# Kernel optimization log

Measured on AMD Instinct MI355X. Metric: run time of the kernel, lower is better.

The kernel has to match this reference:

```python
import jax, jax.numpy as jnp
import numpy as np

SAMPLE_RATE = 24000.0
SIGMA_MULT = 4.0
CHUNK = 512  # atoms processed per scan step (mirrors chunked Triton kernel)


def setup_inputs() -> dict:
    key = jax.random.key(0)
    ks = jax.random.split(key, 6)
    N = 4096
    num_samples = 72000  # 3 seconds at 24kHz
    duration = num_samples / SAMPLE_RATE
    amplitude = 0.1 * jax.random.normal(ks[0], (N,), dtype=jnp.float32)
    tau = jax.random.uniform(ks[1], (N,), dtype=jnp.float32) * duration
    omega = jax.random.uniform(ks[2], (N,), dtype=jnp.float32) * 8000.0
    sigma = 0.002 + jax.random.uniform(ks[3], (N,), dtype=jnp.float32) * 0.020
    phi = jax.random.uniform(ks[4], (N,), dtype=jnp.float32) * (2.0 * np.pi)
    gamma = 500.0 * jax.random.normal(ks[5], (N,), dtype=jnp.float32)
    return {"amplitude": amplitude, "tau": tau, "omega": omega,
            "sigma": sigma, "phi": phi, "gamma": gamma,
            "num_samples": num_samples}


def _render(amplitude, tau, omega, sigma, phi, gamma, num_samples):
    t = jnp.arange(num_samples, dtype=jnp.float32) / SAMPLE_RATE  # [T]
    two_pi = jnp.float32(2.0 * np.pi)

    def chunk_sum(acc, params):
        a, tu, om, sg, ph, gm = params  # each [CHUNK]
        tc = t[None, :] - tu[:, None]                    # [C,T]
        mask = jnp.abs(tc) <= SIGMA_MULT * sg[:, None]
        env = jnp.exp(-tc * tc / (2.0 * sg[:, None] ** 2 + 1e-8))
        phase = two_pi * (om[:, None] * tc + 0.5 * gm[:, None] * tc * tc) + ph[:, None]
        atoms = a[:, None] * env * jnp.cos(phase) * mask.astype(jnp.float32)
        return acc + atoms.sum(axis=0), None

    N = amplitude.shape[0]
    rs = lambda x: x.reshape(N // CHUNK, CHUNK)
    params = (rs(amplitude), rs(tau), rs(omega), rs(sigma), rs(phi), rs(gamma))
    out, _ = jax.lax.scan(chunk_sum, jnp.zeros((num_samples,), jnp.float32), params)
    return out


def reference(amplitude, tau, omega, sigma, phi, gamma, num_samples):
    return _render(amplitude, tau, omega, sigma, phi, gamma, num_samples)
```

## Files before the change

### kernel.cpp

```cpp
#include <hip/hip_runtime.h>
#include <math.h>


#define SR         24000.0f
#define TWO_PI     6.2831853071795864769f
#define LOG2E      1.4426950408889634f

#define TS     512
#define RBLOCK 128
#define SPT    4
#define SEGS   8
#define MAXA   512

__global__ __launch_bounds__(64) void prep_kernel(
        const float* __restrict__ tau,
        const float* __restrict__ sigma,
        int*   __restrict__ counts,
        int*   __restrict__ lists,
        float* __restrict__ out,
        int N, int T, int ntiles) {
    const int b    = blockIdx.x;
    const int lane = threadIdx.x;

    if (b < ntiles) {
        const float tstart = (float)(b * TS) * (1.0f / SR);
        const float tend   = (float)(b * TS + TS - 1) * (1.0f / SR);
        const float slack  = 2.0f / SR;
        int cnt = 0;
        for (int c = 0; c < N; c += 64) {
            const int ai = c + lane;
            bool hit = false;
            if (ai < N) {
                const float tu = tau[ai];
                const float w  = 4.0f * sigma[ai] + slack;
                hit = ((tu - w) <= tend) && ((tu + w) >= tstart);
            }
            const unsigned long long m = __ballot(hit);
            if (hit) {
                const int pos = cnt + (int)__popcll(m & ((1ull << lane) - 1ull));
                if (pos < MAXA) lists[b * MAXA + pos] = ai;
            }
            cnt += (int)__popcll(m);
        }
        if (lane == 0) counts[b] = (cnt < MAXA) ? cnt : MAXA;
    } else {
        const int i4 = (b - ntiles) * 64 + lane;
        if (i4 * 4 < T) ((float4*)out)[i4] = make_float4(0.f, 0.f, 0.f, 0.f);
    }
}

__global__ __launch_bounds__(RBLOCK) void render_kernel(
        const float* __restrict__ amp,
        const float* __restrict__ tau,
        const float* __restrict__ omega,
        const float* __restrict__ sigma,
        const float* __restrict__ phi,
        const float* __restrict__ gamma,
        const int*   __restrict__ counts,
        const int*   __restrict__ lists,
        float*       __restrict__ out,
        int T) {
    __shared__ float4 s_par[RBLOCK][2];

    const int tile = blockIdx.x;
    const int seg  = blockIdx.y;
    const int tid  = threadIdx.x;
    const int s_base = tile * TS;
    const float t0 = (float)(s_base + tid) * (1.0f / SR);
    const float dt = (float)RBLOCK * (1.0f / SR);

    int cnt = counts[tile];
    const int per = (cnt + SEGS - 1) / SEGS;
    const int a0 = seg * per;
    const int a1 = min(cnt, a0 + per);

    const int* lst = lists + tile * MAXA;
    float acc[SPT] = {0.0f, 0.0f, 0.0f, 0.0f};

    for (int base = a0; base < a1; base += RBLOCK) {
        const int m = min(RBLOCK, a1 - base);
        __syncthreads();
        if (tid < m) {
            const int idx = lst[base + tid];
            const float a  = amp[idx];
            const float tu = tau[idx];
            const float om = omega[idx];
            const float sg = sigma[idx];
            const float ph = phi[idx];
            const float gm = gamma[idx];
            const float k  = -LOG2E / (2.0f * sg * sg + 1e-8f);
            s_par[tid][0] = make_float4(a, tu, om, 0.5f * gm);
            s_par[tid][1] = make_float4(k, ph * (1.0f / TWO_PI), 0.0f, 0.0f);
        }
        __syncthreads();

        for (int i = 0; i < m; ++i) {
            const float4 p0 = s_par[i][0];
            const float4 p1 = s_par[i][1];
            const float tc0 = t0 - p0.y;
            #pragma unroll
            for (int j = 0; j < SPT; ++j) {
                const float tc  = tc0 + (float)j * dt;
                const float tc2 = tc * tc;
                const float env = exp2f(p1.x * tc2);
                const float rev = fmaf(p0.z, tc, fmaf(p0.w, tc2, p1.y));
                const float r   = rev - floorf(rev);
                const float c   = __builtin_amdgcn_cosf(r);
                acc[j] = fmaf(p0.x * env, c, acc[j]);
            }
        }
    }

    #pragma unroll
    for (int j = 0; j < SPT; ++j) {
        const int t_idx = s_base + tid + j * RBLOCK;
        if (t_idx < T && a1 > a0) atomicAdd(&out[t_idx], acc[j]);
    }
}

extern "C" void kernel_launch(void* const* d_in, const int* in_sizes, int n_in,
                              void* d_out, int out_size, void* d_ws, size_t ws_size,
                              hipStream_t stream) {
    const float* amp   = (const float*)d_in[0];
    const float* tau   = (const float*)d_in[1];
    const float* omega = (const float*)d_in[2];
    const float* sigma = (const float*)d_in[3];
    const float* phi   = (const float*)d_in[4];
    const float* gamma = (const float*)d_in[5];

    float* out = (float*)d_out;
    const int T = out_size;
    const int N = in_sizes[0];
    const int ntiles = (T + TS - 1) / TS;

    char* ws = (char*)d_ws;
    int* counts = (int*)ws;
    int* lists  = (int*)(ws + (size_t)ntiles * sizeof(int));

    const int zblocks = (T / 4 + 63) / 64;
    prep_kernel<<<ntiles + zblocks, 64, 0, stream>>>(tau, sigma, counts, lists,
                                                     out, N, T, ntiles);
    dim3 grid(ntiles, SEGS);
    render_kernel<<<grid, RBLOCK, 0, stream>>>(amp, tau, omega, sigma, phi, gamma,
                                               counts, lists, out, T);
}
```

Before: 95.94 us.

## Fuse atom binning and rendering into one kernel without atomics

Merges the prep (per-tile atom culling plus output zeroing) and render kernels into one kernel. Each 512-thread block culls all atoms for its tile with a block-wide ballot and prefix sum into shared memory, loads parameters, then has each thread render one sample and write it directly. This drops the second launch, the global lists buffer, the output zeroing and the atomicAdds. In exchange each tile's atom list is no longer split across 8 segment blocks, so only about 141 blocks run, each scanning all N atoms serially with barriers per chunk.

```diff
diff --git a/kernel.cpp b/kernel.cpp
--- a/kernel.cpp
+++ b/kernel.cpp
@@ -2,120 +2,96 @@
 #include <math.h>
 
 
-#define SR         24000.0f
-#define TWO_PI     6.2831853071795864769f
-#define LOG2E      1.4426950408889634f
+#define SR      24000.0f
+#define TWO_PI  6.2831853071795864769f
+#define LOG2E   1.4426950408889634f
 
-#define TS     512
-#define RBLOCK 128
-#define SPT    4
-#define SEGS   8
-#define MAXA   512
+#define TS      512
+#define BLK     512
+#define NWAVES  (BLK / 64)
+#define MAXA    512
 
-__global__ __launch_bounds__(64) void prep_kernel(
-        const float* __restrict__ tau,
-        const float* __restrict__ sigma,
-        int*   __restrict__ counts,
-        int*   __restrict__ lists,
-        float* __restrict__ out,
-        int N, int T, int ntiles) {
-    const int b    = blockIdx.x;
-    const int lane = threadIdx.x;
-
-    if (b < ntiles) {
-        const float tstart = (float)(b * TS) * (1.0f / SR);
-        const float tend   = (float)(b * TS + TS - 1) * (1.0f / SR);
-        const float slack  = 2.0f / SR;
-        int cnt = 0;
-        for (int c = 0; c < N; c += 64) {
-            const int ai = c + lane;
-            bool hit = false;
-            if (ai < N) {
-                const float tu = tau[ai];
-                const float w  = 4.0f * sigma[ai] + slack;
-                hit = ((tu - w) <= tend) && ((tu + w) >= tstart);
-            }
-            const unsigned long long m = __ballot(hit);
-            if (hit) {
-                const int pos = cnt + (int)__popcll(m & ((1ull << lane) - 1ull));
-                if (pos < MAXA) lists[b * MAXA + pos] = ai;
-            }
-            cnt += (int)__popcll(m);
-        }
-        if (lane == 0) counts[b] = (cnt < MAXA) ? cnt : MAXA;
-    } else {
-        const int i4 = (b - ntiles) * 64 + lane;
-        if (i4 * 4 < T) ((float4*)out)[i4] = make_float4(0.f, 0.f, 0.f, 0.f);
-    }
-}
-
-__global__ __launch_bounds__(RBLOCK) void render_kernel(
+__global__ __launch_bounds__(BLK) void gabor_fused_kernel(
         const float* __restrict__ amp,
         const float* __restrict__ tau,
         const float* __restrict__ omega,
         const float* __restrict__ sigma,
         const float* __restrict__ phi,
         const float* __restrict__ gamma,
-        const int*   __restrict__ counts,
-        const int*   __restrict__ lists,
         float*       __restrict__ out,
-        int T) {
-    __shared__ float4 s_par[RBLOCK][2];
+        int N, int T) {
+    __shared__ int    s_list[MAXA];
+    __shared__ int    s_wcnt[NWAVES];
+    __shared__ float4 s_p4[MAXA];
+    __shared__ float2 s_p2[MAXA];
 
     const int tile = blockIdx.x;
-    const int seg  = blockIdx.y;
     const int tid  = threadIdx.x;
-    const int s_base = tile * TS;
-    const float t0 = (float)(s_base + tid) * (1.0f / SR);
-    const float dt = (float)RBLOCK * (1.0f / SR);
+    const int wid  = tid >> 6;
+    const int lane = tid & 63;
 
-    int cnt = counts[tile];
-    const int per = (cnt + SEGS - 1) / SEGS;
-    const int a0 = seg * per;
-    const int a1 = min(cnt, a0 + per);
+    const float tstart = (float)(tile * TS) * (1.0f / SR);
+    const float tend   = (float)(tile * TS + TS - 1) * (1.0f / SR);
+    const float slack  = 2.0f / SR;
 
-    const int* lst = lists + tile * MAXA;
-    float acc[SPT] = {0.0f, 0.0f, 0.0f, 0.0f};
+    int total = 0;
+    for (int c = 0; c < N; c += BLK) {
+        const int ai = c + tid;
+        bool hit = false;
+        if (ai < N) {
+            const float tu = tau[ai];
+            const float w  = 4.0f * sigma[ai] + slack;
+            hit = ((tu - w) <= tend) && ((tu + w) >= tstart);
+        }
+        const unsigned long long m = __ballot(hit);
+        if (lane == 0) s_wcnt[wid] = (int)__popcll(m);
+        __syncthreads();
 
-    for (int base = a0; base < a1; base += RBLOCK) {
-        const int m = min(RBLOCK, a1 - base);
-        __syncthreads();
-        if (tid < m) {
-            const int idx = lst[base + tid];
-            const float a  = amp[idx];
-            const float tu = tau[idx];
-            const float om = omega[idx];
-            const float sg = sigma[idx];
-            const float ph = phi[idx];
-            const float gm = gamma[idx];
-            const float k  = -LOG2E / (2.0f * sg * sg + 1e-8f);
-            s_par[tid][0] = make_float4(a, tu, om, 0.5f * gm);
-            s_par[tid][1] = make_float4(k, ph * (1.0f / TWO_PI), 0.0f, 0.0f);
+        int off = total;
+        #pragma unroll
+        for (int w2 = 0; w2 < NWAVES; ++w2) {
+            const int c2 = s_wcnt[w2];
+            if (w2 < wid) off += c2;
+            total += c2;
+        }
+        if (hit) {
+            const int pos = off + (int)__popcll(m & ((1ull << lane) - 1ull));
+            if (pos < MAXA) s_list[pos] = ai;
         }
         __syncthreads();
+    }
+    const int cnt = (total < MAXA) ? total : MAXA;
 
-        for (int i = 0; i < m; ++i) {
-            const float4 p0 = s_par[i][0];
-            const float4 p1 = s_par[i][1];
-            const float tc0 = t0 - p0.y;
-            #pragma unroll
-            for (int j = 0; j < SPT; ++j) {
-                const float tc  = tc0 + (float)j * dt;
-                const float tc2 = tc * tc;
-                const float env = exp2f(p1.x * tc2);
-                const float rev = fmaf(p0.z, tc, fmaf(p0.w, tc2, p1.y));
-                const float r   = rev - floorf(rev);
-                const float c   = __builtin_amdgcn_cosf(r);
-                acc[j] = fmaf(p0.x * env, c, acc[j]);
-            }
-        }
+    if (tid < cnt) {
+        const int idx = s_list[tid];
+        const float a  = amp[idx];
+        const float tu = tau[idx];
+        const float om = omega[idx];
+        const float sg = sigma[idx];
+        const float ph = phi[idx];
+        const float gm = gamma[idx];
+        const float k  = -LOG2E / (2.0f * sg * sg + 1e-8f);
+        s_p4[tid] = make_float4(a, om, 0.5f * gm, k);
+        s_p2[tid] = make_float2(tu, ph * (1.0f / TWO_PI));
     }
+    __syncthreads();
 
-    #pragma unroll
-    for (int j = 0; j < SPT; ++j) {
-        const int t_idx = s_base + tid + j * RBLOCK;
-        if (t_idx < T && a1 > a0) atomicAdd(&out[t_idx], acc[j]);
+    const int   t_idx = tile * TS + tid;
+    const float t0    = (float)t_idx * (1.0f / SR);
+    float acc = 0.0f;
+    #pragma unroll 4
+    for (int i = 0; i < cnt; ++i) {
+        const float4 p4 = s_p4[i];
+        const float2 p2 = s_p2[i];
+        const float tc  = t0 - p2.x;
+        const float tc2 = tc * tc;
+        const float env = exp2f(p4.w * tc2);
+        const float rev = fmaf(p4.y, tc, fmaf(p4.z, tc2, p2.y));
+        const float r   = rev - floorf(rev);
+        const float c   = __builtin_amdgcn_cosf(r);
+        acc = fmaf(p4.x * env, c, acc);
     }
+    if (t_idx < T) out[t_idx] = acc;
 }
 
 extern "C" void kernel_launch(void* const* d_in, const int* in_sizes, int n_in,
@@ -133,14 +109,8 @@
     const int N = in_sizes[0];
     const int ntiles = (T + TS - 1) / TS;
 
-    char* ws = (char*)d_ws;
-    int* counts = (int*)ws;
-    int* lists  = (int*)(ws + (size_t)ntiles * sizeof(int));
+    (void)d_ws; (void)ws_size;
 
-    const int zblocks = (T / 4 + 63) / 64;
-    prep_kernel<<<ntiles + zblocks, 64, 0, stream>>>(tau, sigma, counts, lists,
-                                                     out, N, T, ntiles);
-    dim3 grid(ntiles, SEGS);
-    render_kernel<<<grid, RBLOCK, 0, stream>>>(amp, tau, omega, sigma, phi, gamma,
-                                               counts, lists, out, T);
+    gabor_fused_kernel<<<ntiles, BLK, 0, stream>>>(amp, tau, omega, sigma, phi,
+                                                   gamma, out, N, T);
 }
```

Result: faster. 82.87 us (-13.6%).
